# Kernel optimization log

Hardware: AMD Instinct MI355X
Metric: run time of the kernel (lower is better)

The kernel has to match this reference:

```python
import jax, jax.numpy as jnp
import numpy as np


def get_rel_pos(q_size, k_size, rel_pos):
    # table length == 2*max(q,k)-1, so no interpolation branch is needed.
    # relative coords: i - j + (k_size - 1) (q_size == k_size here)
    coords = jnp.arange(q_size)[:, None] - jnp.arange(k_size)[None, :] + (k_size - 1)
    return rel_pos[coords]  # (q_size, k_size, head_dim)


def setup_inputs() -> dict:
    key = jax.random.key(0)
    ks = jax.random.split(key, 11)
    B, H, W, C = 4, 32, 32, 768
    nH, d = 12, 64
    L = 2 * H - 1
    s = 0.02
    return {
        "x": jax.random.normal(ks[0], (B, H, W, C), jnp.float32),
        "Wq": jax.random.normal(ks[1], (nH, d, C), jnp.float32) * s,
        "Wk": jax.random.normal(ks[2], (nH, d, C), jnp.float32) * s,
        "Wv": jax.random.normal(ks[3], (nH, d, C), jnp.float32) * s,
        "bq": jax.random.normal(ks[4], (nH, d), jnp.float32) * s,
        "bk": jax.random.normal(ks[5], (nH, d), jnp.float32) * s,
        "bv": jax.random.normal(ks[6], (nH, d), jnp.float32) * s,
        "rel_pos_h": jax.random.normal(ks[7], (L, d), jnp.float32) * s,
        "rel_pos_w": jax.random.normal(ks[8], (L, d), jnp.float32) * s,
        "proj_w": jax.random.normal(ks[9], (C, C), jnp.float32) * s,
        "proj_b": jax.random.normal(ks[10], (C,), jnp.float32) * s,
    }


def reference(x, Wq, Wk, Wv, bq, bk, bv, rel_pos_h, rel_pos_w, proj_w, proj_b):
    B, H, W, C = x.shape
    nH, d, _ = Wq.shape
    scale = d ** -0.5
    S = H * W

    # Per-head 1x1-conv QKV projection (split-head loop in the original ==
    # one batched einsum over the head axis; same math).
    q = jnp.einsum('bhwc,ndc->bnhwd', x, Wq) + bq[None, :, None, None, :]
    k = jnp.einsum('bhwc,ndc->bnhwd', x, Wk) + bk[None, :, None, None, :]
    v = jnp.einsum('bhwc,ndc->bnhwd', x, Wv) + bv[None, :, None, None, :]

    qf = q.reshape(B, nH, S, d)
    kf = k.reshape(B, nH, S, d)
    vf = v.reshape(B, nH, S, d)

    # (q * scale) @ k^T -> (B, nH, S, S)
    attn = jnp.einsum('bnqd,bnkd->bnqk', qf * scale, kf)

    # Decomposed relative position bias
    Rh = get_rel_pos(H, H, rel_pos_h)  # (H, H, d)
    Rw = get_rel_pos(W, W, rel_pos_w)  # (W, W, d)
    rel_h = jnp.einsum('bnhwd,hkd->bnhwk', q, Rh)  # (B, nH, H, W, k_h)
    rel_w = jnp.einsum('bnhwd,wkd->bnhwk', q, Rw)  # (B, nH, H, W, k_w)
    attn = (attn.reshape(B, nH, H, W, H, W)
            + rel_h[:, :, :, :, :, None]
            + rel_w[:, :, :, :, None, :]).reshape(B, nH, S, S)

    attn = jax.nn.softmax(attn, axis=-1)
    out = jnp.einsum('bnqk,bnkd->bnqd', attn, vf)  # (B, nH, S, d)
    # concat heads: (B, nH, H, W, d) -> (B, H, W, nH*d)
    out = out.reshape(B, nH, H, W, d).transpose(0, 2, 3, 1, 4).reshape(B, H, W, nH * d)
    # output projection (1x1 conv == linear)
    return out @ proj_w.T + proj_b
```

## Files before the change

### kernel.cpp

```cpp
#include <hip/hip_runtime.h>
#include <hip/hip_bf16.h>
#include <math.h>

typedef float4 f4;
typedef __attribute__((ext_vector_type(8))) short bf16x8;
typedef __attribute__((ext_vector_type(4))) float f32x4;
typedef __attribute__((ext_vector_type(16))) float f32x16;

#define CD   768
#define SEQ  1024
#define NHD  12
#define DH   64

__device__ __forceinline__ ushort f2bf(float x) {
    union { __hip_bfloat16 h; ushort u; } v;
    v.h = __float2bfloat16(x);
    return v.u;
}
__device__ __forceinline__ unsigned pk2bf(float a, float b) {
    union { __hip_bfloat162 h; unsigned u; } v;
    v.h = __float22bfloat162_rn(make_float2(a, b));
    return v.u;
}
__device__ __forceinline__ void gload_lds16(const ushort* g, ushort* l) {
    __builtin_amdgcn_global_load_lds((const __attribute__((address_space(1))) void*)g,
                                     (__attribute__((address_space(3))) void*)l, 16, 0, 0);
}

__global__ __launch_bounds__(256) void cvt_bf16_k(
    const float* __restrict__ x, const float* __restrict__ Wq,
    const float* __restrict__ Wk, const float* __restrict__ Wv,
    const float* __restrict__ pw, ushort* __restrict__ dst)
{
    const int idx = blockIdx.x * 256 + threadIdx.x;
    if (idx >= 1376256) return;
    const int e = idx << 2;
    if (e < 4915200) {
        const float* src; int off;
        if      (e < 3145728) { src = x;  off = e; }
        else if (e < 3735552) { src = Wq; off = e - 3145728; }
        else if (e < 4325376) { src = Wk; off = e - 3735552; }
        else                  { src = Wv; off = e - 4325376; }
        const f4 v = *(const f4*)(src + off);
        uint2 o;
        o.x = pk2bf(v.x, v.y);
        o.y = pk2bf(v.z, v.w);
        *(uint2*)(dst + e) = o;
    } else {
        const int off = e - 4915200;
        const int n = off / CD, k = off - n * CD;
        const f4 v = *(const f4*)(pw + off);
        uint2 o;
        o.x = pk2bf(v.x, v.y);
        o.y = pk2bf(v.z, v.w);
        *(uint2*)(dst + 4915200 + ((size_t)(k >> 6) * CD + n) * 64 + (k & 63)) = o;
    }
}

__global__ __launch_bounds__(256, 2) void qkv_mfma(
    const ushort* __restrict__ xbf,
    const ushort* __restrict__ wq, const ushort* __restrict__ wk, const ushort* __restrict__ wv,
    const float* __restrict__ bq, const float* __restrict__ bk, const float* __restrict__ bv,
    ushort* __restrict__ qbf, ushort* __restrict__ kbf, ushort* __restrict__ vbfT)
{
    __shared__ __align__(16) ushort Sq[32768];

    const int t = threadIdx.x;
    const int w = t >> 6, l = t & 63;
    const int lr = l & 15, lg = l >> 4;
    const int n0 = blockIdx.x << 7;
    const int m0 = blockIdx.y << 7;
    const int sel  = n0 / CD;
    const int nloc = n0 % CD;
    const ushort* Wb  = (sel == 0) ? wq : ((sel == 1) ? wk : wv);
    const float* bias = (sel == 0) ? bq : ((sel == 1) ? bk : bv);

    const int srow = (w << 3) + (l >> 3);
    const int scol = (l & 7) << 3;
    const ushort* Agl = xbf + (size_t)(m0 + srow) * CD + scol;
    const ushort* Bgl = Wb + (size_t)(nloc + srow) * CD + scol;

    f32x4 acc[4][4];
    #pragma unroll
    for (int mi = 0; mi < 4; ++mi)
        #pragma unroll
        for (int ni = 0; ni < 4; ++ni) acc[mi][ni] = (f32x4){0.f, 0.f, 0.f, 0.f};

    const int mb = (w >> 1) << 6, nb = (w & 1) << 6;

    #pragma unroll
    for (int i = 0; i < 4; ++i) {
        gload_lds16(Agl + (size_t)(i << 5) * CD, &Sq[(i << 11) + (w << 9)]);
        gload_lds16(Bgl + (size_t)(i << 5) * CD, &Sq[8192 + (i << 11) + (w << 9)]);
    }
    __syncthreads();

    for (int kt = 0; kt < 12; ++kt) {
        const int cb = (kt & 1) << 14;
        if (kt < 11) {
            const int nbuf = ((kt + 1) & 1) << 14;
            const int kc = (kt + 1) << 6;
            #pragma unroll
            for (int i = 0; i < 4; ++i) {
                gload_lds16(Agl + (size_t)(i << 5) * CD + kc, &Sq[nbuf + (i << 11) + (w << 9)]);
                gload_lds16(Bgl + (size_t)(i << 5) * CD + kc, &Sq[nbuf + 8192 + (i << 11) + (w << 9)]);
            }
        }
        #pragma unroll
        for (int kk = 0; kk < 2; ++kk) {
            bf16x8 af[4], bf[4];
            #pragma unroll
            for (int mi = 0; mi < 4; ++mi)
                af[mi] = *(const bf16x8*)&Sq[cb + (mb + (mi << 4) + lr) * 64 + (kk << 5) + (lg << 3)];
            #pragma unroll
            for (int ni = 0; ni < 4; ++ni)
                bf[ni] = *(const bf16x8*)&Sq[cb + 8192 + (nb + (ni << 4) + lr) * 64 + (kk << 5) + (lg << 3)];
            #pragma unroll
            for (int mi = 0; mi < 4; ++mi)
                #pragma unroll
                for (int ni = 0; ni < 4; ++ni)
                    acc[mi][ni] = __builtin_amdgcn_mfma_f32_16x16x32_bf16(af[mi], bf[ni], acc[mi][ni], 0, 0, 0);
        }
        __syncthreads();
    }

    ushort* Ep = Sq + (w << 12);

    float bl[4];
    #pragma unroll
    for (int ni = 0; ni < 4; ++ni) bl[ni] = bias[nloc + nb + (ni << 4) + lr];

    if (sel < 2) {
        #pragma unroll
        for (int mi = 0; mi < 4; ++mi)
            #pragma unroll
            for (int ni = 0; ni < 4; ++ni)
                #pragma unroll
                for (int reg = 0; reg < 4; ++reg)
                    Ep[((mi << 4) + (lg << 2) + reg) * 64 + (ni << 4) + lr] =
                        f2bf(acc[mi][ni][reg] + bl[ni]);
    } else {
        #pragma unroll
        for (int mi = 0; mi < 4; ++mi)
            #pragma unroll
            for (int ni = 0; ni < 4; ++ni)
                #pragma unroll
                for (int reg = 0; reg < 4; ++reg)
                    Ep[((ni << 4) + lr) * 64 + (lg << 4) + (reg << 2) + mi] =
                        f2bf(acc[mi][ni][reg] + bl[ni]);
    }

    const int bi   = m0 >> 10;
    const int si0  = (m0 & 1023) + mb;
    const int head = (nloc + nb) >> 6;
    const int bn   = bi * NHD + head;
    const ushort* src = Ep + l * 64;
    if (sel < 2) {
        ushort* dbf = (sel == 0) ? qbf : kbf;
        ushort* dst = dbf + (((size_t)bn << 10) + si0 + l) * 64;
        #pragma unroll
        for (int c = 0; c < 8; ++c)
            *(bf16x8*)(dst + (c << 3)) = *(const bf16x8*)(src + (c << 3));
    } else {
        ushort* dst = vbfT + (((size_t)(bn * DH + l)) << 10) + si0;
        #pragma unroll
        for (int c = 0; c < 8; ++c)
            *(bf16x8*)(dst + (c << 3)) = *(const bf16x8*)(src + (c << 3));
    }
}

__global__ __launch_bounds__(256, 4) void rel_kernel(
    const ushort* __restrict__ qbf, const float* __restrict__ rph,
    const float* __restrict__ rpw,
    float* __restrict__ rhb2, float* __restrict__ rwb)
{
    __shared__ float Pl[4][64][33];

    const int t = threadIdx.x;
    const int w = t >> 6, l = t & 63;
    const int q5 = l & 31, g = l >> 5;
    const int hq = blockIdx.x, bn = blockIdx.y;
    const int h = (hq << 2) + w;
    const int s = (h << 5) + q5;

    const ushort* qp = qbf + (((size_t)bn << 10) + s) * 64 + (g << 3);
    bf16x8 qf[4];
    #pragma unroll
    for (int c = 0; c < 4; ++c) qf[c] = *(const bf16x8*)(qp + (c << 4));

    f32x16 acch;
    #pragma unroll
    for (int i = 0; i < 16; ++i) acch[i] = 0.f;
    {
        const float* rp = rph + (size_t)(h + 31 - q5) * 64 + (g << 3);
        #pragma unroll
        for (int c = 0; c < 4; ++c) {
            const f4 v0 = *(const f4*)(rp + (c << 4));
            const f4 v1 = *(const f4*)(rp + (c << 4) + 4);
            union { unsigned u[4]; bf16x8 v; } u;
            u.u[0] = pk2bf(v0.x, v0.y); u.u[1] = pk2bf(v0.z, v0.w);
            u.u[2] = pk2bf(v1.x, v1.y); u.u[3] = pk2bf(v1.z, v1.w);
            acch = __builtin_amdgcn_mfma_f32_32x32x16_bf16(u.v, qf[c], acch, 0, 0, 0);
        }
    }
    {
        float* base = rhb2 + (((size_t)(bn * 16 + (h >> 1)) << 4) << 7)
                    + ((((h & 1) << 5) + q5) << 1);
        #pragma unroll
        for (int r = 0; r < 16; r += 2) {
            const int k2 = (r & 3) + ((r >> 2) << 3) + (g << 2);
            *(float2*)(base + ((size_t)(k2 >> 1) << 7)) = make_float2(acch[r], acch[r + 1]);
        }
    }

    f32x16 accw[2];
    #pragma unroll
    for (int i = 0; i < 16; ++i) { accw[0][i] = 0.f; accw[1][i] = 0.f; }
    #pragma unroll
    for (int b = 0; b < 2; ++b) {
        const int r = (b << 5) + q5;
        const bool ok = (r < 63);
        const float* rp = rpw + (size_t)r * 64 + (g << 3);
        #pragma unroll
        for (int c = 0; c < 4; ++c) {
            union { unsigned u[4]; bf16x8 v; } u;
            if (ok) {
                const f4 v0 = *(const f4*)(rp + (c << 4));
                const f4 v1 = *(const f4*)(rp + (c << 4) + 4);
                u.u[0] = pk2bf(v0.x, v0.y); u.u[1] = pk2bf(v0.z, v0.w);
                u.u[2] = pk2bf(v1.x, v1.y); u.u[3] = pk2bf(v1.z, v1.w);
            } else {
                u.u[0] = 0u; u.u[1] = 0u; u.u[2] = 0u; u.u[3] = 0u;
            }
            accw[b] = __builtin_amdgcn_mfma_f32_32x32x16_bf16(u.v, qf[c], accw[b], 0, 0, 0);
        }
    }
    #pragma unroll
    for (int b = 0; b < 2; ++b)
        #pragma unroll
        for (int r = 0; r < 16; ++r) {
            const int row = (r & 3) + ((r >> 2) << 3) + (g << 2) + (b << 5);
            Pl[w][row][q5] = accw[b][r];
        }
    __syncthreads();
    float ow[16];
    #pragma unroll
    for (int i = 0; i < 16; ++i) {
        const int k2 = (g << 4) + i;
        ow[i] = Pl[w][q5 + 31 - k2][q5];
    }
    float* wb = rwb + ((((size_t)bn << 10) + s) << 5) + (g << 4);
    #pragma unroll
    for (int i = 0; i < 4; ++i) {
        f4 v; v.x = ow[4*i]; v.y = ow[4*i+1]; v.z = ow[4*i+2]; v.w = ow[4*i+3];
        *(f4*)(wb + (i << 2)) = v;
    }
}

__global__ __launch_bounds__(256, 3) void attn_mfma(
    const ushort* __restrict__ qbf, const ushort* __restrict__ kbf,
    const ushort* __restrict__ vbfT,
    const float* __restrict__ rhb2, const float* __restrict__ rwb,
    ushort* __restrict__ abf2)
{
    __shared__ __align__(16) ushort KV[2][8192];
    __shared__ __align__(16) ushort Pl[4][16][72];

    const int t  = threadIdx.x;
    const int l  = t & 63, w = t >> 6;
    const int lr = l & 15, lg = l >> 4;
    const int qt = blockIdx.x, bn = blockIdx.y;
    const int q0 = qt << 6;

    const ushort* qp = qbf + (((size_t)bn << 10) + q0 + w * 16 + lr) * DH + lg * 8;
    const bf16x8 qa0 = *(const bf16x8*)qp;
    const bf16x8 qa1 = *(const bf16x8*)(qp + 32);

    float rw_[4][2];
    #pragma unroll
    for (int reg = 0; reg < 4; ++reg) {
        const size_t rrow = ((size_t)bn << 10) + q0 + w * 16 + lg * 4 + reg;
        rw_[reg][0] = rwb[(rrow << 5) + lr];
        rw_[reg][1] = rwb[(rrow << 5) + 16 + lr];
    }
    const float* rhbase = rhb2 + (size_t)(bn * 16 + qt) * 2048 + (w * 16 + lg * 4) * 2;

    const int i0   = w << 1;
    const int rsub = l >> 3;
    const int coff = ((l & 7) ^ rsub) << 3;
    const size_t kbase = ((size_t)bn << 16);
    const ushort* kp0 = kbf + kbase + (size_t)((i0 << 3) + rsub) * 64 + coff;
    const ushort* kp1 = kp0 + 512;
    const ushort* vp0 = vbfT + kbase + ((size_t)((i0 << 3) + rsub) << 10) + coff;
    const ushort* vp1 = vp0 + 8192;
    const int lds0 = i0 << 9;

    f32x4 oc[4];
    #pragma unroll
    for (int nf = 0; nf < 4; ++nf) oc[nf] = (f32x4){0.f, 0.f, 0.f, 0.f};
    f32x4 sumc = (f32x4){0.f, 0.f, 0.f, 0.f};
    bf16x8 ones;
    #pragma unroll
    for (int i = 0; i < 8; ++i) ones[i] = (short)0x3F80;

    const int s0c = lg ^ (lr & 7);

    gload_lds16(kp0, &KV[0][lds0]);
    gload_lds16(kp1, &KV[0][lds0 + 512]);
    gload_lds16(vp0, &KV[0][4096 + lds0]);
    gload_lds16(vp1, &KV[0][4096 + lds0 + 512]);
    __syncthreads();

    for (int kt = 0; kt < 16; ++kt) {
        const int cur = kt & 1;
        if (kt < 15) {
            ushort* nb_ = &KV[cur ^ 1][0];
            gload_lds16(kp0 + ((kt + 1) << 12), nb_ + lds0);
            gload_lds16(kp1 + ((kt + 1) << 12), nb_ + lds0 + 512);
            gload_lds16(vp0 + ((kt + 1) << 6), nb_ + 4096 + lds0);
            gload_lds16(vp1 + ((kt + 1) << 6), nb_ + 4096 + lds0 + 512);
        }
        const ushort* Kl = &KV[cur][0];
        const ushort* Vt = &KV[cur][4096];
        const f4 rh01 = *(const f4*)(rhbase + (kt << 7));
        const f4 rh23 = *(const f4*)(rhbase + (kt << 7) + 4);

        f32x4 sc[4];
        #pragma unroll
        for (int f = 0; f < 4; ++f) {
            f32x4 c = (f32x4){0.f, 0.f, 0.f, 0.f};
            const int rb = (f * 16 + lr) * 64;
            const bf16x8 kb0 = *(const bf16x8*)&Kl[rb + (s0c << 3)];
            const bf16x8 kb1 = *(const bf16x8*)&Kl[rb + ((s0c ^ 4) << 3)];
            c = __builtin_amdgcn_mfma_f32_16x16x32_bf16(qa0, kb0, c, 0, 0, 0);
            c = __builtin_amdgcn_mfma_f32_16x16x32_bf16(qa1, kb1, c, 0, 0, 0);
            sc[f] = c;
        }

        #pragma unroll
        for (int reg = 0; reg < 4; ++reg) {
            const float rhx = (reg == 0) ? rh01.x : (reg == 1) ? rh01.z
                             : (reg == 2) ? rh23.x : rh23.z;
            const float rhy = (reg == 0) ? rh01.y : (reg == 1) ? rh01.w
                             : (reg == 2) ? rh23.y : rh23.w;
            const float e0 = __expf(fmaf(sc[0][reg], 0.125f, rhx + rw_[reg][0]));
            const float e1 = __expf(fmaf(sc[1][reg], 0.125f, rhx + rw_[reg][1]));
            const float e2 = __expf(fmaf(sc[2][reg], 0.125f, rhy + rw_[reg][0]));
            const float e3 = __expf(fmaf(sc[3][reg], 0.125f, rhy + rw_[reg][1]));
            uint2 pk;
            pk.x = pk2bf(e0, e1);
            pk.y = pk2bf(e2, e3);
            *(uint2*)&Pl[w][lg * 4 + reg][lr * 4] = pk;
        }

        const bf16x8 pa0 = *(const bf16x8*)&Pl[w][lr][lg * 8];
        const bf16x8 pa1 = *(const bf16x8*)&Pl[w][lr][lg * 8 + 32];
        sumc = __builtin_amdgcn_mfma_f32_16x16x32_bf16(pa0, ones, sumc, 0, 0, 0);
        sumc = __builtin_amdgcn_mfma_f32_16x16x32_bf16(pa1, ones, sumc, 0, 0, 0);
        #pragma unroll
        for (int nf = 0; nf < 4; ++nf) {
            const int rb = (nf * 16 + lr) * 64;
            const bf16x8 vb0 = *(const bf16x8*)&Vt[rb + (s0c << 3)];
            const bf16x8 vb1 = *(const bf16x8*)&Vt[rb + ((s0c ^ 4) << 3)];
            oc[nf] = __builtin_amdgcn_mfma_f32_16x16x32_bf16(pa0, vb0, oc[nf], 0, 0, 0);
            oc[nf] = __builtin_amdgcn_mfma_f32_16x16x32_bf16(pa1, vb1, oc[nf], 0, 0, 0);
        }
        __syncthreads();
    }

    const int bi = bn / NHD, hn = bn - bi * NHD;
    #pragma unroll
    for (int reg = 0; reg < 4; ++reg) {
        const float inv = 1.f / sumc[reg];
        const int row = q0 + w * 16 + lg * 4 + reg;
        ushort* dst = abf2 + ((size_t)hn * 4096 + (bi << 10) + row) * 64 + lr;
        union { unsigned u; ushort2 s2; } a, b;
        a.u = pk2bf(oc[0][reg] * inv, oc[1][reg] * inv);
        b.u = pk2bf(oc[2][reg] * inv, oc[3][reg] * inv);
        dst[0]  = a.s2.x;
        dst[16] = a.s2.y;
        dst[32] = b.s2.x;
        dst[48] = b.s2.y;
    }
}

__global__ __launch_bounds__(256, 2) void proj_mfma(
    const ushort* __restrict__ abf2, const ushort* __restrict__ pwbf2,
    const float* __restrict__ pb, float* __restrict__ out)
{
    __shared__ __align__(16) ushort Sp[32768];

    const int t = threadIdx.x;
    const int w = t >> 6, l = t & 63;
    const int lr = l & 15, lg = l >> 4;
    const int n0 = blockIdx.x << 7;
    const int m0 = blockIdx.y << 7;

    const int srow = (w << 3) + (l >> 3);
    const int scol = (l & 7) << 3;
    const ushort* Agl = abf2 + (size_t)(m0 + srow) * 64 + scol;
    const ushort* Bgl = pwbf2 + (size_t)(n0 + srow) * 64 + scol;

    f32x4 acc[4][4];
    #pragma unroll
    for (int mi = 0; mi < 4; ++mi)
        #pragma unroll
        for (int ni = 0; ni < 4; ++ni) acc[mi][ni] = (f32x4){0.f, 0.f, 0.f, 0.f};

    const int mb = (w >> 1) << 6, nb = (w & 1) << 6;

    #pragma unroll
    for (int i = 0; i < 4; ++i) {
        gload_lds16(Agl + (size_t)(i << 5) * 64, &Sp[(i << 11) + (w << 9)]);
        gload_lds16(Bgl + (size_t)(i << 5) * 64, &Sp[8192 + (i << 11) + (w << 9)]);
    }
    __syncthreads();

    for (int kt = 0; kt < 12; ++kt) {
        const int cb = (kt & 1) << 14;
        if (kt < 11) {
            const int nbuf = ((kt + 1) & 1) << 14;
            #pragma unroll
            for (int i = 0; i < 4; ++i) {
                gload_lds16(Agl + ((size_t)(kt + 1) * 4096 + (i << 5)) * 64,
                            &Sp[nbuf + (i << 11) + (w << 9)]);
                gload_lds16(Bgl + ((size_t)(kt + 1) * CD + (i << 5)) * 64,
                            &Sp[nbuf + 8192 + (i << 11) + (w << 9)]);
            }
        }
        #pragma unroll
        for (int kk = 0; kk < 2; ++kk) {
            bf16x8 af[4], bf[4];
            #pragma unroll
            for (int mi = 0; mi < 4; ++mi)
                af[mi] = *(const bf16x8*)&Sp[cb + (mb + (mi << 4) + lr) * 64 + (kk << 5) + (lg << 3)];
            #pragma unroll
            for (int ni = 0; ni < 4; ++ni)
                bf[ni] = *(const bf16x8*)&Sp[cb + 8192 + (nb + (ni << 4) + lr) * 64 + (kk << 5) + (lg << 3)];
            #pragma unroll
            for (int mi = 0; mi < 4; ++mi)
                #pragma unroll
                for (int ni = 0; ni < 4; ++ni)
                    acc[mi][ni] = __builtin_amdgcn_mfma_f32_16x16x32_bf16(af[mi], bf[ni], acc[mi][ni], 0, 0, 0);
        }
        __syncthreads();
    }

    float bl[4];
    #pragma unroll
    for (int ni = 0; ni < 4; ++ni) bl[ni] = pb[n0 + nb + (ni << 4) + lr];
    #pragma unroll
    for (int mi = 0; mi < 4; ++mi)
        #pragma unroll
        for (int ni = 0; ni < 4; ++ni)
            #pragma unroll
            for (int reg = 0; reg < 4; ++reg)
                out[(size_t)(m0 + mb + (mi << 4) + (lg << 2) + reg) * CD
                    + n0 + nb + (ni << 4) + lr] = acc[mi][ni][reg] + bl[ni];
}

extern "C" void kernel_launch(void* const* d_in, const int* in_sizes, int n_in,
                              void* d_out, int out_size, void* d_ws, size_t ws_size,
                              hipStream_t stream) {
    (void)in_sizes; (void)n_in; (void)out_size; (void)ws_size;
    const float* x   = (const float*)d_in[0];
    const float* Wq  = (const float*)d_in[1];
    const float* Wk  = (const float*)d_in[2];
    const float* Wv  = (const float*)d_in[3];
    const float* bq  = (const float*)d_in[4];
    const float* bk  = (const float*)d_in[5];
    const float* bv  = (const float*)d_in[6];
    const float* rph = (const float*)d_in[7];
    const float* rpw = (const float*)d_in[8];
    const float* pw  = (const float*)d_in[9];
    const float* pb  = (const float*)d_in[10];
    float* out = (float*)d_out;

    ushort* cvt  = (ushort*)d_ws;
    ushort* xbf  = cvt;
    ushort* wqbf = cvt + 3145728;
    ushort* wkbf = wqbf + 589824;
    ushort* wvbf = wkbf + 589824;
    ushort* pwbf = wvbf + 589824;
    ushort* qbf  = pwbf + 589824;
    ushort* kbf  = qbf  + 3145728;
    ushort* vbfT = kbf  + 3145728;
    ushort* abf2 = vbfT + 3145728;
    float*  rhb2 = (float*)(abf2 + 3145728);
    float*  rwb  = rhb2 + 1572864;

    hipLaunchKernelGGL(cvt_bf16_k, dim3(5376), dim3(256), 0, stream,
                       x, Wq, Wk, Wv, pw, cvt);
    hipLaunchKernelGGL(qkv_mfma, dim3(18, 32), dim3(256), 0, stream,
                       xbf, wqbf, wkbf, wvbf, bq, bk, bv, qbf, kbf, vbfT);
    hipLaunchKernelGGL(rel_kernel, dim3(8, 48), dim3(256), 0, stream,
                       qbf, rph, rpw, rhb2, rwb);
    hipLaunchKernelGGL(attn_mfma, dim3(16, 48), dim3(256), 0, stream,
                       qbf, kbf, vbfT, rhb2, rwb, abf2);
    hipLaunchKernelGGL(proj_mfma, dim3(6, 32), dim3(256), 0, stream,
                       abf2, pwbf, pb, out);
}
```

Baseline: 98.47 us.

## Fuse relative-position bias computation into attention kernel prologue

```diff
diff --git a/kernel.cpp b/kernel.cpp
--- a/kernel.cpp
+++ b/kernel.cpp
@@ -169,102 +169,15 @@
     }
 }
 
-__global__ __launch_bounds__(256, 4) void rel_kernel(
-    const ushort* __restrict__ qbf, const float* __restrict__ rph,
-    const float* __restrict__ rpw,
-    float* __restrict__ rhb2, float* __restrict__ rwb)
-{
-    __shared__ float Pl[4][64][33];
-
-    const int t = threadIdx.x;
-    const int w = t >> 6, l = t & 63;
-    const int q5 = l & 31, g = l >> 5;
-    const int hq = blockIdx.x, bn = blockIdx.y;
-    const int h = (hq << 2) + w;
-    const int s = (h << 5) + q5;
-
-    const ushort* qp = qbf + (((size_t)bn << 10) + s) * 64 + (g << 3);
-    bf16x8 qf[4];
-    #pragma unroll
-    for (int c = 0; c < 4; ++c) qf[c] = *(const bf16x8*)(qp + (c << 4));
-
-    f32x16 acch;
-    #pragma unroll
-    for (int i = 0; i < 16; ++i) acch[i] = 0.f;
-    {
-        const float* rp = rph + (size_t)(h + 31 - q5) * 64 + (g << 3);
-        #pragma unroll
-        for (int c = 0; c < 4; ++c) {
-            const f4 v0 = *(const f4*)(rp + (c << 4));
-            const f4 v1 = *(const f4*)(rp + (c << 4) + 4);
-            union { unsigned u[4]; bf16x8 v; } u;
-            u.u[0] = pk2bf(v0.x, v0.y); u.u[1] = pk2bf(v0.z, v0.w);
-            u.u[2] = pk2bf(v1.x, v1.y); u.u[3] = pk2bf(v1.z, v1.w);
-            acch = __builtin_amdgcn_mfma_f32_32x32x16_bf16(u.v, qf[c], acch, 0, 0, 0);
-        }
-    }
-    {
-        float* base = rhb2 + (((size_t)(bn * 16 + (h >> 1)) << 4) << 7)
-                    + ((((h & 1) << 5) + q5) << 1);
-        #pragma unroll
-        for (int r = 0; r < 16; r += 2) {
-            const int k2 = (r & 3) + ((r >> 2) << 3) + (g << 2);
-            *(float2*)(base + ((size_t)(k2 >> 1) << 7)) = make_float2(acch[r], acch[r + 1]);
-        }
-    }
-
-    f32x16 accw[2];
-    #pragma unroll
-    for (int i = 0; i < 16; ++i) { accw[0][i] = 0.f; accw[1][i] = 0.f; }
-    #pragma unroll
-    for (int b = 0; b < 2; ++b) {
-        const int r = (b << 5) + q5;
-        const bool ok = (r < 63);
-        const float* rp = rpw + (size_t)r * 64 + (g << 3);
-        #pragma unroll
-        for (int c = 0; c < 4; ++c) {
-            union { unsigned u[4]; bf16x8 v; } u;
-            if (ok) {
-                const f4 v0 = *(const f4*)(rp + (c << 4));
-                const f4 v1 = *(const f4*)(rp + (c << 4) + 4);
-                u.u[0] = pk2bf(v0.x, v0.y); u.u[1] = pk2bf(v0.z, v0.w);
-                u.u[2] = pk2bf(v1.x, v1.y); u.u[3] = pk2bf(v1.z, v1.w);
-            } else {
-                u.u[0] = 0u; u.u[1] = 0u; u.u[2] = 0u; u.u[3] = 0u;
-            }
-            accw[b] = __builtin_amdgcn_mfma_f32_32x32x16_bf16(u.v, qf[c], accw[b], 0, 0, 0);
-        }
-    }
-    #pragma unroll
-    for (int b = 0; b < 2; ++b)
-        #pragma unroll
-        for (int r = 0; r < 16; ++r) {
-            const int row = (r & 3) + ((r >> 2) << 3) + (g << 2) + (b << 5);
-            Pl[w][row][q5] = accw[b][r];
-        }
-    __syncthreads();
-    float ow[16];
-    #pragma unroll
-    for (int i = 0; i < 16; ++i) {
-        const int k2 = (g << 4) + i;
-        ow[i] = Pl[w][q5 + 31 - k2][q5];
-    }
-    float* wb = rwb + ((((size_t)bn << 10) + s) << 5) + (g << 4);
-    #pragma unroll
-    for (int i = 0; i < 4; ++i) {
-        f4 v; v.x = ow[4*i]; v.y = ow[4*i+1]; v.z = ow[4*i+2]; v.w = ow[4*i+3];
-        *(f4*)(wb + (i << 2)) = v;
-    }
-}
-
 __global__ __launch_bounds__(256, 3) void attn_mfma(
     const ushort* __restrict__ qbf, const ushort* __restrict__ kbf,
     const ushort* __restrict__ vbfT,
-    const float* __restrict__ rhb2, const float* __restrict__ rwb,
+    const float* __restrict__ rph, const float* __restrict__ rpw,
     ushort* __restrict__ abf2)
 {
     __shared__ __align__(16) ushort KV[2][8192];
     __shared__ __align__(16) ushort Pl[4][16][72];
+    __shared__ __align__(16) float rhs_[2048];
 
     const int t  = threadIdx.x;
     const int l  = t & 63, w = t >> 6;
@@ -272,18 +185,109 @@
     const int qt = blockIdx.x, bn = blockIdx.y;
     const int q0 = qt << 6;
 
+    {
+        const int p   = w >> 1;
+        const int sub = w & 1;
+        const int h   = (qt << 1) + p;
+        const int q5  = l & 31, g = l >> 5;
+
+        const ushort* qp = qbf + (((size_t)bn << 10) + (h << 5) + q5) * 64 + (g << 3);
+        bf16x8 qf[4];
+        #pragma unroll
+        for (int c = 0; c < 4; ++c) qf[c] = *(const bf16x8*)(qp + (c << 4));
+
+        float* PwF = (float*)&KV[0][0] + p * 2112;
+
+        if (sub == 0) {
+            f32x16 acch;
+            #pragma unroll
+            for (int i = 0; i < 16; ++i) acch[i] = 0.f;
+            {
+                const float* rp = rph + (size_t)(h + 31 - q5) * 64 + (g << 3);
+                #pragma unroll
+                for (int c = 0; c < 4; ++c) {
+                    const f4 v0 = *(const f4*)(rp + (c << 4));
+                    const f4 v1 = *(const f4*)(rp + (c << 4) + 4);
+                    union { unsigned u[4]; bf16x8 v; } u;
+                    u.u[0] = pk2bf(v0.x, v0.y); u.u[1] = pk2bf(v0.z, v0.w);
+                    u.u[2] = pk2bf(v1.x, v1.y); u.u[3] = pk2bf(v1.z, v1.w);
+                    acch = __builtin_amdgcn_mfma_f32_32x32x16_bf16(u.v, qf[c], acch, 0, 0, 0);
+                }
+            }
+            #pragma unroll
+            for (int r = 0; r < 16; r += 2) {
+                const int k2 = (r & 3) + ((r >> 2) << 3) + (g << 2);
+                *(float2*)&rhs_[((k2 >> 1) << 7) + (((p << 5) + q5) << 1)] =
+                    make_float2(acch[r], acch[r + 1]);
+            }
+            f32x16 accw;
+            #pragma unroll
+            for (int i = 0; i < 16; ++i) accw[i] = 0.f;
+            {
+                const float* rp = rpw + (size_t)q5 * 64 + (g << 3);
+                #pragma unroll
+                for (int c = 0; c < 4; ++c) {
+                    const f4 v0 = *(const f4*)(rp + (c << 4));
+                    const f4 v1 = *(const f4*)(rp + (c << 4) + 4);
+                    union { unsigned u[4]; bf16x8 v; } u;
+                    u.u[0] = pk2bf(v0.x, v0.y); u.u[1] = pk2bf(v0.z, v0.w);
+                    u.u[2] = pk2bf(v1.x, v1.y); u.u[3] = pk2bf(v1.z, v1.w);
+                    accw = __builtin_amdgcn_mfma_f32_32x32x16_bf16(u.v, qf[c], accw, 0, 0, 0);
+                }
+            }
+            #pragma unroll
+            for (int r = 0; r < 16; ++r) {
+                const int row = (r & 3) + ((r >> 2) << 3) + (g << 2);
+                PwF[row * 33 + q5] = accw[r];
+            }
+        } else {
+            f32x16 accw;
+            #pragma unroll
+            for (int i = 0; i < 16; ++i) accw[i] = 0.f;
+            {
+                const bool ok = (32 + q5) < 63;
+                const float* rp = rpw + (size_t)(32 + q5) * 64 + (g << 3);
+                #pragma unroll
+                for (int c = 0; c < 4; ++c) {
+                    union { unsigned u[4]; bf16x8 v; } u;
+                    if (ok) {
+                        const f4 v0 = *(const f4*)(rp + (c << 4));
+                        const f4 v1 = *(const f4*)(rp + (c << 4) + 4);
+                        u.u[0] = pk2bf(v0.x, v0.y); u.u[1] = pk2bf(v0.z, v0.w);
+                        u.u[2] = pk2bf(v1.x, v1.y); u.u[3] = pk2bf(v1.z, v1.w);
+                    } else {
+                        u.u[0] = 0u; u.u[1] = 0u; u.u[2] = 0u; u.u[3] = 0u;
+                    }
+                    accw = __builtin_amdgcn_mfma_f32_32x32x16_bf16(u.v, qf[c], accw, 0, 0, 0);
+                }
+            }
+            #pragma unroll
+            for (int r = 0; r < 16; ++r) {
+                const int row = (r & 3) + ((r >> 2) << 3) + (g << 2) + 32;
+                PwF[row * 33 + q5] = accw[r];
+            }
+        }
+    }
+    __syncthreads();
+
+    float rw_[4][2];
+    {
+        const int p = w >> 1;
+        const float* PwF = (float*)&KV[0][0] + p * 2112;
+        #pragma unroll
+        for (int reg = 0; reg < 4; ++reg) {
+            const int q5w = ((w & 1) << 4) + (lg << 2) + reg;
+            rw_[reg][0] = PwF[(q5w + 31 - lr) * 33 + q5w];
+            rw_[reg][1] = PwF[(q5w + 15 - lr) * 33 + q5w];
+        }
+    }
+    __syncthreads();
+
     const ushort* qp = qbf + (((size_t)bn << 10) + q0 + w * 16 + lr) * DH + lg * 8;
     const bf16x8 qa0 = *(const bf16x8*)qp;
     const bf16x8 qa1 = *(const bf16x8*)(qp + 32);
 
-    float rw_[4][2];
-    #pragma unroll
-    for (int reg = 0; reg < 4; ++reg) {
-        const size_t rrow = ((size_t)bn << 10) + q0 + w * 16 + lg * 4 + reg;
-        rw_[reg][0] = rwb[(rrow << 5) + lr];
-        rw_[reg][1] = rwb[(rrow << 5) + 16 + lr];
-    }
-    const float* rhbase = rhb2 + (size_t)(bn * 16 + qt) * 2048 + (w * 16 + lg * 4) * 2;
+    const int rhbase = ((w * 16 + lg * 4) << 1);
 
     const int i0   = w << 1;
     const int rsub = l >> 3;
@@ -322,8 +326,8 @@
         }
         const ushort* Kl = &KV[cur][0];
         const ushort* Vt = &KV[cur][4096];
-        const f4 rh01 = *(const f4*)(rhbase + (kt << 7));
-        const f4 rh23 = *(const f4*)(rhbase + (kt << 7) + 4);
+        const f4 rh01 = *(const f4*)&rhs_[(kt << 7) + rhbase];
+        const f4 rh23 = *(const f4*)&rhs_[(kt << 7) + rhbase + 4];
 
         f32x4 sc[4];
         #pragma unroll
@@ -486,17 +490,13 @@
     ushort* kbf  = qbf  + 3145728;
     ushort* vbfT = kbf  + 3145728;
     ushort* abf2 = vbfT + 3145728;
-    float*  rhb2 = (float*)(abf2 + 3145728);
-    float*  rwb  = rhb2 + 1572864;
 
     hipLaunchKernelGGL(cvt_bf16_k, dim3(5376), dim3(256), 0, stream,
                        x, Wq, Wk, Wv, pw, cvt);
     hipLaunchKernelGGL(qkv_mfma, dim3(18, 32), dim3(256), 0, stream,
                        xbf, wqbf, wkbf, wvbf, bq, bk, bv, qbf, kbf, vbfT);
-    hipLaunchKernelGGL(rel_kernel, dim3(8, 48), dim3(256), 0, stream,
-                       qbf, rph, rpw, rhb2, rwb);
     hipLaunchKernelGGL(attn_mfma, dim3(16, 48), dim3(256), 0, stream,
-                       qbf, kbf, vbfT, rhb2, rwb, abf2);
+                       qbf, kbf, vbfT, rph, rpw, abf2);
     hipLaunchKernelGGL(proj_mfma, dim3(6, 32), dim3(256), 0, stream,
                        abf2, pwbf, pb, out);
 }
```

After: 88.83 us. -9.8%, faster.
